# Kernel optimization log

Hardware: AMD Instinct MI355X
Metric: run time of the kernel (lower is better)

## Reference

```python
import jax, jax.numpy as jnp
import numpy as np

N, E, H, NH = 10000, 160000, 128, 8
HD = H // NH
LDIM = 8  # (lmax+1)**2 - 1 with lmax=2
CUTOFF = 5.0


def setup_inputs() -> dict:
    key = jax.random.key(0)
    ks = jax.random.split(key, 20)
    w = lambda k, shape: jax.random.normal(k, shape, jnp.float32) * 0.05
    return dict(
        node_feats=jax.random.normal(ks[0], (N, H), jnp.float32),
        edge_feats=jax.random.normal(ks[1], (E, H), jnp.float32),
        vector_feats=jax.random.normal(ks[2], (N, LDIM, H), jnp.float32),
        distances=jax.random.uniform(ks[3], (E,), jnp.float32) * CUTOFF,
        d_ij=jax.random.normal(ks[4], (E, LDIM), jnp.float32),
        senders=jax.random.randint(ks[5], (E,), 0, N),
        receivers=jax.random.randint(ks[6], (E,), 0, N),
        ln_scale=jnp.ones((H,), jnp.float32),
        ln_bias=jnp.zeros((H,), jnp.float32),
        vln_w=jnp.ones((H,), jnp.float32),
        W_vec=w(ks[7], (H, 3 * H)),
        Wq=w(ks[8], (H, H)), bq=jnp.zeros((H,), jnp.float32),
        Wk=w(ks[9], (H, H)), bk=jnp.zeros((H,), jnp.float32),
        Wv=w(ks[10], (H, H)), bv=jnp.zeros((H,), jnp.float32),
        Wdk=w(ks[11], (H, H)), bdk=jnp.zeros((H,), jnp.float32),
        Wdv=w(ks[12], (H, H)), bdv=jnp.zeros((H,), jnp.float32),
        Ws=w(ks[13], (H, 2 * H)), bs=jnp.zeros((2 * H,), jnp.float32),
        Wo=w(ks[14], (H, 3 * H)), bo=jnp.zeros((3 * H,), jnp.float32),
        Wf=w(ks[15], (H, H)), bf=jnp.zeros((H,), jnp.float32),
        Wsrc=w(ks[16], (H, H)),
        Wtrg=w(ks[17], (H, H)),
    )


def _reject(vec, d):
    # vector rejection of vec [E, L, H] against direction d [E, L]
    proj = (vec * d[:, :, None]).sum(axis=1, keepdims=True)
    return vec - proj * d[:, :, None]


def _forward(node_feats, edge_feats, vector_feats, distances, d_ij, senders, receivers,
             ln_scale, ln_bias, vln_w, W_vec, Wq, bq, Wk, bk, Wv, bv, Wdk, bdk, Wdv, bdv,
             Ws, bs, Wo, bo, Wf, bf, Wsrc, Wtrg):
    silu = jax.nn.silu
    n = node_feats.shape[0]
    # LayerNorm (eps=1e-5) on node feats
    mu = node_feats.mean(-1, keepdims=True)
    xc = node_feats - mu
    var = (xc * xc).mean(-1, keepdims=True)
    x = xc * jax.lax.rsqrt(var + 1e-5) * ln_scale + ln_bias
    # VecLayerNorm with norm_type='none' -> identity norm + learned per-channel scale
    vec = vector_feats * vln_w
    q = (x @ Wq + bq).reshape(-1, NH, HD)
    k = (x @ Wk + bk).reshape(-1, NH, HD)
    v = (x @ Wv + bv).reshape(-1, NH, HD)
    dk = silu(edge_feats @ Wdk + bdk).reshape(-1, NH, HD)
    dv = silu(edge_feats @ Wdv + bdv).reshape(-1, NH, HD)
    vec1, vec2, vec3 = jnp.split(vec @ W_vec, [H, 2 * H], axis=-1)
    vec_dot = (vec1 * vec2).sum(axis=1)  # [N, H]
    # per-edge gathers
    q_i = q[receivers]
    k_j = k[senders]
    v_j = v[senders]
    vec_j = vec[senders]  # [E, LDIM, H]
    # attention-style message with cosine cutoff
    cut = 0.5 * (jnp.cos(distances * (jnp.pi / CUTOFF)) + 1.0) * (distances < CUTOFF)
    attn = silu((q_i * k_j * dk).sum(-1)) * cut[:, None]  # [E, NH]
    vj = ((v_j * dv) * attn[:, :, None]).reshape(-1, H)   # [E, H]
    s1, s2 = jnp.split(silu(vj @ Ws + bs), [H], axis=1)
    vec_msg = vec_j * s1[:, None, :] + s2[:, None, :] * d_ij[:, :, None]
    # scatter reduce to nodes
    node_agg = jax.ops.segment_sum(vj, receivers, num_segments=n)
    vec_agg = jax.ops.segment_sum(vec_msg, receivers, num_segments=n)
    o1, o2, o3 = jnp.split(node_agg @ Wo + bo, [H, 2 * H], axis=1)
    dx = vec_dot * o2 + o3
    dvec = vec3 * o1[:, None, :] + vec_agg
    # edge update (last_layer=False)
    w1 = _reject(vec[receivers] @ Wtrg, d_ij)
    w2 = _reject(vec_j @ Wsrc, -d_ij)
    w_dot = (w1 * w2).sum(axis=1)  # [E, H]
    df_ij = silu(edge_feats @ Wf + bf) * w_dot
    return dx, df_ij, dvec


def reference(node_feats, edge_feats, vector_feats, distances, d_ij, senders, receivers,
              ln_scale, ln_bias, vln_w, W_vec, Wq, bq, Wk, bk, Wv, bv, Wdk, bdk, Wdv, bdv,
              Ws, bs, Wo, bo, Wf, bf, Wsrc, Wtrg):
    return _forward(node_feats, edge_feats, vector_feats, distances, d_ij, senders, receivers,
                    ln_scale, ln_bias, vln_w, W_vec, Wq, bq, Wk, bk, Wv, bv, Wdk, bdk, Wdv, bdv,
                    Ws, bs, Wo, bo, Wf, bf, Wsrc, Wtrg)
```

## Files before the change

### kernel.cpp

```cpp
#include <hip/hip_runtime.h>
#include <math.h>

#define NN 10000
#define NE 160000
#define H  128
#define LD 8

typedef unsigned short ushort_t;
typedef short bf16x8 __attribute__((ext_vector_type(8)));
typedef float f32x4 __attribute__((ext_vector_type(4)));

__device__ __forceinline__ float silu_f(float x){ return x / (1.0f + expf(-x)); }
__device__ __forceinline__ float4 f4z(){ return make_float4(0.f,0.f,0.f,0.f); }

__device__ __forceinline__ void fma4(float4& acc, float s, const float4 w){
    acc.x = fmaf(s, w.x, acc.x);
    acc.y = fmaf(s, w.y, acc.y);
    acc.z = fmaf(s, w.z, acc.z);
    acc.w = fmaf(s, w.w, acc.w);
}

__device__ __forceinline__ float4 silu4(float4 a, float4 b){
    return make_float4(silu_f(a.x+b.x), silu_f(a.y+b.y), silu_f(a.z+b.z), silu_f(a.w+b.w));
}

__device__ __forceinline__ ushort_t f2bf(float f){
    union { float f; unsigned int u; } x; x.f = f;
    unsigned int r = x.u + 0x7FFFu + ((x.u >> 16) & 1u);
    return (ushort_t)(r >> 16);
}
__device__ __forceinline__ unsigned int pack2bf(float a, float b){
    return (unsigned int)f2bf(a) | ((unsigned int)f2bf(b) << 16);
}
__device__ __forceinline__ float bf2f_hi(unsigned int u){
    union { unsigned int u; float f; } x; x.u = u & 0xffff0000u; return x.f;
}
__device__ __forceinline__ float bf2f_lo(unsigned int u){
    union { unsigned int u; float f; } x; x.u = u << 16; return x.f;
}

__global__ void k_prepw(const float* __restrict__ Wdk, const float* __restrict__ Wdv,
                        const float* __restrict__ Ws,
                        ushort_t* __restrict__ wdkT, ushort_t* __restrict__ wdvT,
                        ushort_t* __restrict__ wsT){
    int i = blockIdx.x * 256 + threadIdx.x;
    if (i < 128*128){
        int n = i >> 7, kk = i & 127;
        wdkT[n*128 + kk] = f2bf(Wdk[kk*128 + n]);
        wdvT[n*128 + kk] = f2bf(Wdv[kk*128 + n]);
    }
    if (i < 256*128){
        int n = i >> 7, kk = i & 127;
        wsT[n*128 + kk] = f2bf(Ws[kk*256 + n]);
    }
}

__global__ void k_ef2bf(const float* __restrict__ ef, ushort_t* __restrict__ ef_bf){
    size_t i = (size_t)blockIdx.x * 256 + threadIdx.x;
    const float4* s = (const float4*)ef;
    float4 a = s[2*i], b = s[2*i+1];
    uint4 u;
    u.x = pack2bf(a.x, a.y); u.y = pack2bf(a.z, a.w);
    u.z = pack2bf(b.x, b.y); u.w = pack2bf(b.z, b.w);
    ((uint4*)ef_bf)[i] = u;
}

__global__ void k_hist(const int* __restrict__ rcv, int* __restrict__ cnt){
    int e = blockIdx.x * 256 + threadIdx.x;
    if (e < NE) atomicAdd(&cnt[rcv[e]], 1);
}

__global__ __launch_bounds__(256) void k_scan(const int* __restrict__ cnt, int* __restrict__ offs){
    __shared__ int part[256];
    const int t = threadIdx.x;
    const int CH = 40;
    int loc[CH];
    int base = t * CH;
    int lsum = 0;
    if (base < NN){
        #pragma unroll
        for (int i = 0; i < CH; i++){ loc[i] = cnt[base + i]; lsum += loc[i]; }
    }
    part[t] = lsum;
    __syncthreads();
    for (int off = 1; off < 256; off <<= 1){
        int v = (t >= off) ? part[t - off] : 0;
        __syncthreads();
        part[t] += v;
        __syncthreads();
    }
    int ex = part[t] - lsum;
    if (base < NN){
        int run = ex;
        #pragma unroll
        for (int i = 0; i < CH; i++){ offs[base + i] = run; run += loc[i]; }
    }
    if (t == 255) offs[NN] = part[255];
}

__global__ void k_scatter(const int* __restrict__ rcv, const int* __restrict__ offs,
                          int* __restrict__ cnt2, int* __restrict__ eidx){
    int e = blockIdx.x * 256 + threadIdx.x;
    if (e < NE){
        int r = rcv[e];
        int p = atomicAdd(&cnt2[r], 1);
        eidx[offs[r] + p] = e;
    }
}

__global__ __launch_bounds__(128) void node_pre(
    const float* __restrict__ nf, const float* __restrict__ vf,
    const float* __restrict__ ln_s, const float* __restrict__ ln_b,
    const float* __restrict__ vlnw, const float* __restrict__ W_vec,
    const float* __restrict__ Wq, const float* __restrict__ bq,
    const float* __restrict__ Wk, const float* __restrict__ bk,
    const float* __restrict__ Wv, const float* __restrict__ bv,
    const float* __restrict__ Wtrg, const float* __restrict__ Wsrc,
    float* __restrict__ q, float* __restrict__ k, float* __restrict__ v,
    ushort_t* __restrict__ vec_bf, float* __restrict__ vdot, float* __restrict__ vec3,
    ushort_t* __restrict__ Vt, ushort_t* __restrict__ Vs)
{
    const int n = blockIdx.x;
    const int h = threadIdx.x;
    __shared__ float x_s[H];
    __shared__ float vec_s[LD][H];
    __shared__ float red[4];

    float xv = nf[(size_t)n*H + h];
    float s1 = xv, s2 = xv*xv;
    #pragma unroll
    for (int o = 32; o >= 1; o >>= 1){
        s1 += __shfl_xor(s1, o, 64);
        s2 += __shfl_xor(s2, o, 64);
    }
    const int wid = h >> 6;
    if ((h & 63) == 0){ red[wid] = s1; red[2+wid] = s2; }
    __syncthreads();
    float mean = (red[0] + red[1]) * (1.0f/H);
    float var  = (red[2] + red[3]) * (1.0f/H) - mean*mean;
    float x = (xv - mean) * rsqrtf(var + 1e-5f) * ln_s[h] + ln_b[h];
    x_s[h] = x;
    float w = vlnw[h];
    #pragma unroll
    for (int l = 0; l < LD; l++){
        size_t i = ((size_t)n*LD + l)*H + h;
        float t = vf[i] * w;
        vec_s[l][h] = t;
        vec_bf[i] = f2bf(t);
    }
    __syncthreads();

    float aq = bq[h], ak = bk[h], av = bv[h];
    float a1[LD], a2[LD], a3[LD], at[LD], as_[LD];
    #pragma unroll
    for (int l = 0; l < LD; l++){ a1[l]=0.f; a2[l]=0.f; a3[l]=0.f; at[l]=0.f; as_[l]=0.f; }

    for (int kk = 0; kk < H; kk++){
        float xk = x_s[kk];
        aq = fmaf(xk, Wq[kk*H + h], aq);
        ak = fmaf(xk, Wk[kk*H + h], ak);
        av = fmaf(xk, Wv[kk*H + h], av);
        float w1 = W_vec[kk*(3*H) + h];
        float w2 = W_vec[kk*(3*H) + H + h];
        float w3 = W_vec[kk*(3*H) + 2*H + h];
        float wt = Wtrg[kk*H + h];
        float ws = Wsrc[kk*H + h];
        #pragma unroll
        for (int l = 0; l < LD; l++){
            float vk = vec_s[l][kk];
            a1[l] = fmaf(vk, w1, a1[l]);
            a2[l] = fmaf(vk, w2, a2[l]);
            a3[l] = fmaf(vk, w3, a3[l]);
            at[l] = fmaf(vk, wt, at[l]);
            as_[l]= fmaf(vk, ws, as_[l]);
        }
    }
    q[(size_t)n*H + h] = aq;
    k[(size_t)n*H + h] = ak;
    v[(size_t)n*H + h] = av;
    float vd = 0.f;
    #pragma unroll
    for (int l = 0; l < LD; l++) vd = fmaf(a1[l], a2[l], vd);
    vdot[(size_t)n*H + h] = vd;
    #pragma unroll
    for (int l = 0; l < LD; l++){
        size_t i = ((size_t)n*LD + l)*H + h;
        vec3[i] = a3[l];
        Vt[i]   = f2bf(at[l]);
        Vs[i]   = f2bf(as_[l]);
    }
}

__global__ __launch_bounds__(256) void edge_attn(
    const ushort_t* __restrict__ ef_bf,
    const ushort_t* __restrict__ wdkT, const float* __restrict__ bdk,
    const ushort_t* __restrict__ wdvT, const float* __restrict__ bdv,
    const int* __restrict__ snd, const int* __restrict__ rcv,
    const float* __restrict__ dist,
    const float* __restrict__ q, const float* __restrict__ k, const float* __restrict__ v,
    ushort_t* __restrict__ vj)
{
    __shared__ ushort_t dk_s[64][136];
    __shared__ ushort_t dv_s[64][136];

    const int tid  = threadIdx.x;
    const int lane = tid & 63;
    const int m0   = (tid >> 6) * 16;
    const size_t e0 = (size_t)blockIdx.x * 64;

    const int mrow = lane & 15;
    const int kblk = lane >> 4;

    f32x4 accK[8], accV[8];
    #pragma unroll
    for (int nt = 0; nt < 8; nt++){ accK[nt] = (f32x4)(0.f); accV[nt] = (f32x4)(0.f); }

    const ushort_t* Arow = ef_bf + (e0 + m0 + mrow)*H + kblk*8;
    const ushort_t* wkb  = wdkT + (size_t)mrow*H + kblk*8;
    const ushort_t* wvb  = wdvT + (size_t)mrow*H + kblk*8;

    #pragma unroll
    for (int ks = 0; ks < 4; ks++){
        bf16x8 a = *(const bf16x8*)(Arow + ks*32);
        #pragma unroll
        for (int nt = 0; nt < 8; nt++){
            bf16x8 bk8 = *(const bf16x8*)(wkb + (size_t)nt*16*H + ks*32);
            accK[nt] = __builtin_amdgcn_mfma_f32_16x16x32_bf16(a, bk8, accK[nt], 0, 0, 0);
            bf16x8 bv8 = *(const bf16x8*)(wvb + (size_t)nt*16*H + ks*32);
            accV[nt] = __builtin_amdgcn_mfma_f32_16x16x32_bf16(a, bv8, accV[nt], 0, 0, 0);
        }
    }

    const int lrow = m0 + 4*kblk;
    #pragma unroll
    for (int nt = 0; nt < 8; nt++){
        int coln = nt*16 + mrow;
        float bkn = bdk[coln], bvn = bdv[coln];
        #pragma unroll
        for (int r = 0; r < 4; r++){
            dk_s[lrow + r][coln] = f2bf(silu_f(accK[nt][r] + bkn));
            dv_s[lrow + r][coln] = f2bf(silu_f(accV[nt][r] + bvn));
        }
    }
    __syncthreads();

    const int r  = tid >> 2, cq = tid & 3;
    const size_t e = e0 + r;
    const int s  = snd[e], rr = rcv[e];
    const float d = dist[e];
    const float cut = (d < 5.0f) ? 0.5f*(cosf(d*0.6283185307179586f) + 1.0f) : 0.0f;
    const float* qrow = q + (size_t)rr*H + cq*32;
    const float* krow = k + (size_t)s*H + cq*32;
    const float* vrow = v + (size_t)s*H + cq*32;
    ushort_t* vjrow = vj + e*H + cq*32;

    #pragma unroll
    for (int hh = 0; hh < 2; hh++){
        const int c0 = hh*16;
        float p = 0.f;
        #pragma unroll
        for (int j = 0; j < 4; j++){
            float4 q4 = *(const float4*)(qrow + c0 + 4*j);
            float4 k4 = *(const float4*)(krow + c0 + 4*j);
            uint2 du = *(const uint2*)&dk_s[r][cq*32 + c0 + 4*j];
            p += q4.x*k4.x*bf2f_lo(du.x) + q4.y*k4.y*bf2f_hi(du.x)
               + q4.z*k4.z*bf2f_lo(du.y) + q4.w*k4.w*bf2f_hi(du.y);
        }
        float attn = silu_f(p) * cut;
        #pragma unroll
        for (int j = 0; j < 4; j++){
            float4 v4 = *(const float4*)(vrow + c0 + 4*j);
            uint2 du = *(const uint2*)&dv_s[r][cq*32 + c0 + 4*j];
            uint2 u;
            u.x = pack2bf(v4.x*bf2f_lo(du.x)*attn, v4.y*bf2f_hi(du.x)*attn);
            u.y = pack2bf(v4.z*bf2f_lo(du.y)*attn, v4.w*bf2f_hi(du.y)*attn);
            *(uint2*)(vjrow + c0 + 4*j) = u;
        }
    }
}

__global__ __launch_bounds__(256) void edge_s(
    const ushort_t* __restrict__ vj, const ushort_t* __restrict__ wsT,
    const float* __restrict__ bs, ushort_t* __restrict__ s12)
{
    __shared__ ushort_t s_s[64][264];

    const int tid  = threadIdx.x;
    const int lane = tid & 63;
    const int m0   = (tid >> 6) * 16;
    const size_t e0 = (size_t)blockIdx.x * 64;

    const int mrow = lane & 15;
    const int kblk = lane >> 4;

    f32x4 acc[16];
    #pragma unroll
    for (int nt = 0; nt < 16; nt++) acc[nt] = (f32x4)(0.f);

    const ushort_t* Arow = vj + (e0 + m0 + mrow)*H + kblk*8;
    const ushort_t* wb   = wsT + (size_t)mrow*H + kblk*8;

    #pragma unroll
    for (int ks = 0; ks < 4; ks++){
        bf16x8 a = *(const bf16x8*)(Arow + ks*32);
        #pragma unroll
        for (int nt = 0; nt < 16; nt++){
            bf16x8 b8 = *(const bf16x8*)(wb + (size_t)nt*16*H + ks*32);
            acc[nt] = __builtin_amdgcn_mfma_f32_16x16x32_bf16(a, b8, acc[nt], 0, 0, 0);
        }
    }

    const int lrow = m0 + 4*kblk;
    #pragma unroll
    for (int nt = 0; nt < 16; nt++){
        int coln = nt*16 + mrow;
        float bb = bs[coln];
        #pragma unroll
        for (int r = 0; r < 4; r++)
            s_s[lrow + r][coln] = f2bf(silu_f(acc[nt][r] + bb));
    }
    __syncthreads();

    const int r = tid >> 2, cq = tid & 3;
    const uint4* srcp = (const uint4*)&s_s[r][cq*64];
    uint4* dstp = (uint4*)&s12[(e0 + r)*256 + cq*64];
    #pragma unroll
    for (int j = 0; j < 8; j++) dstp[j] = srcp[j];
}

__global__ __launch_bounds__(256) void edge_df(
    const float* __restrict__ ef, const float* __restrict__ Wf, const float* __restrict__ bf_,
    const int* __restrict__ eidx,
    const int* __restrict__ snd, const int* __restrict__ rcv,
    const float* __restrict__ dij,
    const ushort_t* __restrict__ Vt, const ushort_t* __restrict__ Vs,
    float* __restrict__ df)
{
    __shared__ float wf_s[H][64];
    __shared__ float e_s[16][H];
    __shared__ int   eidx_s[16];
    __shared__ int   snd_s[16];
    __shared__ int   rcv_s[16];
    __shared__ float dij_s[16][LD];

    const int tid = threadIdx.x;
    const int by = blockIdx.y;
    const int p0 = blockIdx.x * 16;

    if (tid < 16) eidx_s[tid] = eidx[p0 + tid];
    __syncthreads();

    for (int i = tid; i < H*16; i += 256){
        int row = i >> 4, c4 = i & 15;
        *(float4*)&wf_s[row][c4*4] = *(const float4*)&Wf[row*H + by*64 + c4*4];
    }
    for (int i = tid; i < 16*32; i += 256){
        int row = i >> 5, c4 = i & 31;
        *(float4*)&e_s[row][c4*4] = *(const float4*)&ef[(size_t)eidx_s[row]*H + c4*4];
    }
    if (tid < 16){ snd_s[tid] = snd[eidx_s[tid]]; rcv_s[tid] = rcv[eidx_s[tid]]; }
    if (tid < 16*LD){
        int row = tid >> 3, l = tid & 7;
        dij_s[row][l] = dij[(size_t)eidx_s[row]*LD + l];
    }
    __syncthreads();

    const int g = tid & 15, r0 = tid >> 4;
    float4 af = f4z();
    for (int kk = 0; kk < H; kk++){
        float4 w4 = *(float4*)&wf_s[kk][g*4];
        fma4(af, e_s[r0][kk], w4);
    }
    float4 bf4 = *(const float4*)&bf_[by*64 + g*4];
    float4 f4 = silu4(af, bf4);

    const int e = eidx_s[r0];
    const int s = snd_s[r0], rr = rcv_s[r0];
    const ushort_t* Ar = Vt + ((size_t)rr*LD)*H + by*64 + g*4;
    const ushort_t* Br = Vs + ((size_t)s*LD)*H + by*64 + g*4;

    float4 AB = f4z(), aa = f4z(), bb = f4z();
    float dd = 0.f;
    #pragma unroll
    for (int l = 0; l < LD; l++){
        float dl = dij_s[r0][l];
        dd = fmaf(dl, dl, dd);
        uint2 ua = *(const uint2*)&Ar[(size_t)l*H];
        uint2 ub = *(const uint2*)&Br[(size_t)l*H];
        float Ax = bf2f_lo(ua.x), Ay = bf2f_hi(ua.x), Az = bf2f_lo(ua.y), Aw = bf2f_hi(ua.y);
        float Bx = bf2f_lo(ub.x), By = bf2f_hi(ub.x), Bz = bf2f_lo(ub.y), Bw = bf2f_hi(ub.y);
        AB.x = fmaf(Ax, Bx, AB.x); AB.y = fmaf(Ay, By, AB.y);
        AB.z = fmaf(Az, Bz, AB.z); AB.w = fmaf(Aw, Bw, AB.w);
        aa.x = fmaf(Ax, dl, aa.x); aa.y = fmaf(Ay, dl, aa.y);
        aa.z = fmaf(Az, dl, aa.z); aa.w = fmaf(Aw, dl, aa.w);
        bb.x = fmaf(Bx, dl, bb.x); bb.y = fmaf(By, dl, bb.y);
        bb.z = fmaf(Bz, dl, bb.z); bb.w = fmaf(Bw, dl, bb.w);
    }
    float c = 2.0f - dd;
    float4 o = make_float4(f4.x*(AB.x - aa.x*bb.x*c),
                           f4.y*(AB.y - aa.y*bb.y*c),
                           f4.z*(AB.z - aa.z*bb.z*c),
                           f4.w*(AB.w - aa.w*bb.w*c));
    *(float4*)&df[(size_t)e*H + by*64 + g*4] = o;
}

__global__ __launch_bounds__(128) void node_gather(
    const int* __restrict__ offs, const int* __restrict__ eidx, const int* __restrict__ snd,
    const ushort_t* __restrict__ vj, const ushort_t* __restrict__ s12,
    const float* __restrict__ dij, const ushort_t* __restrict__ vec,
    const float* __restrict__ Wo, const float* __restrict__ bo,
    const float* __restrict__ vdot, const float* __restrict__ vec3,
    float* __restrict__ dx, float* __restrict__ dvec)
{
    const int n = blockIdx.x, h = threadIdx.x;
    const int beg = offs[n], end = offs[n+1];
    float na = 0.f;
    float av[LD];
    #pragma unroll
    for (int l = 0; l < LD; l++) av[l] = 0.f;

    for (int i = beg; i < end; i++){
        int e = eidx[i];
        int s = snd[e];
        float vjv = bf2f_lo((unsigned int)vj[(size_t)e*H + h]);
        float s1 = bf2f_lo((unsigned int)s12[(size_t)e*256 + h]);
        float s2 = bf2f_lo((unsigned int)s12[(size_t)e*256 + 128 + h]);
        na += vjv;
        float4 d0 = *(const float4*)&dij[(size_t)e*LD];
        float4 d1 = *(const float4*)&dij[(size_t)e*LD + 4];
        const ushort_t* vr = &vec[(size_t)s*LD*H + h];
        av[0] = fmaf(bf2f_lo((unsigned int)vr[0*H]), s1, fmaf(d0.x, s2, av[0]));
        av[1] = fmaf(bf2f_lo((unsigned int)vr[1*H]), s1, fmaf(d0.y, s2, av[1]));
        av[2] = fmaf(bf2f_lo((unsigned int)vr[2*H]), s1, fmaf(d0.z, s2, av[2]));
        av[3] = fmaf(bf2f_lo((unsigned int)vr[3*H]), s1, fmaf(d0.w, s2, av[3]));
        av[4] = fmaf(bf2f_lo((unsigned int)vr[4*H]), s1, fmaf(d1.x, s2, av[4]));
        av[5] = fmaf(bf2f_lo((unsigned int)vr[5*H]), s1, fmaf(d1.y, s2, av[5]));
        av[6] = fmaf(bf2f_lo((unsigned int)vr[6*H]), s1, fmaf(d1.z, s2, av[6]));
        av[7] = fmaf(bf2f_lo((unsigned int)vr[7*H]), s1, fmaf(d1.w, s2, av[7]));
    }

    __shared__ float na_s[H];
    na_s[h] = na;
    __syncthreads();
    float o1 = bo[h], o2 = bo[H + h], o3 = bo[2*H + h];
    for (int kk = 0; kk < H; kk++){
        float a = na_s[kk];
        o1 = fmaf(a, Wo[kk*(3*H) + h], o1);
        o2 = fmaf(a, Wo[kk*(3*H) + H + h], o2);
        o3 = fmaf(a, Wo[kk*(3*H) + 2*H + h], o3);
    }
    dx[(size_t)n*H + h] = fmaf(vdot[(size_t)n*H + h], o2, o3);
    #pragma unroll
    for (int l = 0; l < LD; l++){
        size_t i2 = ((size_t)n*LD + l)*H + h;
        dvec[i2] = fmaf(vec3[i2], o1, av[l]);
    }
}

extern "C" void kernel_launch(void* const* d_in, const int* in_sizes, int n_in,
                              void* d_out, int out_size, void* d_ws, size_t ws_size,
                              hipStream_t stream) {
    const float* nf    = (const float*)d_in[0];
    const float* ef    = (const float*)d_in[1];
    const float* vf    = (const float*)d_in[2];
    const float* dist  = (const float*)d_in[3];
    const float* dij   = (const float*)d_in[4];
    const int*   snd   = (const int*)d_in[5];
    const int*   rcv   = (const int*)d_in[6];
    const float* ln_s  = (const float*)d_in[7];
    const float* ln_b  = (const float*)d_in[8];
    const float* vlnw  = (const float*)d_in[9];
    const float* W_vec = (const float*)d_in[10];
    const float* Wq    = (const float*)d_in[11];
    const float* bq    = (const float*)d_in[12];
    const float* Wk    = (const float*)d_in[13];
    const float* bk    = (const float*)d_in[14];
    const float* Wv    = (const float*)d_in[15];
    const float* bv    = (const float*)d_in[16];
    const float* Wdk   = (const float*)d_in[17];
    const float* bdk   = (const float*)d_in[18];
    const float* Wdv   = (const float*)d_in[19];
    const float* bdv   = (const float*)d_in[20];
    const float* Ws    = (const float*)d_in[21];
    const float* bs    = (const float*)d_in[22];
    const float* Wo    = (const float*)d_in[23];
    const float* bo    = (const float*)d_in[24];
    const float* Wf    = (const float*)d_in[25];
    const float* bf_   = (const float*)d_in[26];
    const float* Wsrc  = (const float*)d_in[27];
    const float* Wtrg  = (const float*)d_in[28];

    float* out  = (float*)d_out;
    float* dx   = out;
    float* df   = out + (size_t)NN*H;
    float* dvec = df + (size_t)NE*H;

    float* w = (float*)d_ws;
    size_t off = 0;
    float* q    = w + off; off += (size_t)NN*H;
    float* k    = w + off; off += (size_t)NN*H;
    float* v    = w + off; off += (size_t)NN*H;
    float* vdot = w + off; off += (size_t)NN*H;
    float* vec3 = w + off; off += (size_t)NN*LD*H;
    ushort_t* vec_bf = (ushort_t*)(w + off); off += (size_t)NN*LD*H/2;
    ushort_t* Vt     = (ushort_t*)(w + off); off += (size_t)NN*LD*H/2;
    ushort_t* Vs     = (ushort_t*)(w + off); off += (size_t)NN*LD*H/2;
    ushort_t* vj     = (ushort_t*)(w + off); off += (size_t)NE*H/2;
    ushort_t* s12    = (ushort_t*)(w + off); off += (size_t)NE*256/2;
    ushort_t* ef_bf  = s12;
    ushort_t* wdkT = (ushort_t*)(w + off); off += 128*128/2;
    ushort_t* wdvT = (ushort_t*)(w + off); off += 128*128/2;
    ushort_t* wsT  = (ushort_t*)(w + off); off += 256*128/2;
    int* cnt  = (int*)(w + off); off += NN;
    int* cnt2 = (int*)(w + off); off += NN;
    int* offs = (int*)(w + off); off += NN + 1;
    int* eidx = (int*)(w + off); off += NE;

    hipMemsetAsync(cnt,  0, NN*sizeof(int), stream);
    hipMemsetAsync(cnt2, 0, NN*sizeof(int), stream);

    k_prepw<<<128, 256, 0, stream>>>(Wdk, Wdv, Ws, wdkT, wdvT, wsT);
    k_ef2bf<<<NE*H/8/256, 256, 0, stream>>>(ef, ef_bf);

    k_hist<<<(NE+255)/256, 256, 0, stream>>>(rcv, cnt);
    k_scan<<<1, 256, 0, stream>>>(cnt, offs);
    k_scatter<<<(NE+255)/256, 256, 0, stream>>>(rcv, offs, cnt2, eidx);

    node_pre<<<NN, 128, 0, stream>>>(nf, vf, ln_s, ln_b, vlnw, W_vec,
                                     Wq, bq, Wk, bk, Wv, bv, Wtrg, Wsrc,
                                     q, k, v, vec_bf, vdot, vec3, Vt, Vs);

    edge_attn<<<NE/64, 256, 0, stream>>>(ef_bf, wdkT, bdk, wdvT, bdv, snd, rcv, dist,
                                         q, k, v, vj);

    edge_df<<<dim3(NE/16, 2), 256, 0, stream>>>(ef, Wf, bf_, eidx, snd, rcv, dij, Vt, Vs, df);

    edge_s<<<NE/64, 256, 0, stream>>>(vj, wsT, bs, s12);

    node_gather<<<NN, 128, 0, stream>>>(offs, eidx, snd, vj, s12, dij, vec_bf,
                                        Wo, bo, vdot, vec3, dx, dvec);
}
```

Baseline: 910.7 us.

## Split node_pre into LayerNorm plus bf16 MFMA GEMMs for QKV and vector projections

Replaces the per-node scalar FP32 projection kernel with a LayerNorm/scaling kernel that emits bf16, followed by two MFMA GEMM kernels: one for Q/K/V and one for the concatenated W_vec/Wtrg/Wsrc projections, with weights pre-transposed to bf16. The vdot reduction is computed from MFMA accumulators via a lane shuffle, and vec3 is stored as bf16 through a shared-memory staging tile. This removes the heavy scalar FMA loop that re-read weights from global memory for every node. In exchange it lowers Q/K/V and vec3 precision to bf16 and adds extra kernel launches.

```diff
diff --git a/kernel.cpp b/kernel.cpp
--- a/kernel.cpp
+++ b/kernel.cpp
@@ -39,19 +39,38 @@
     union { unsigned int u; float f; } x; x.u = u << 16; return x.f;
 }
 
-__global__ void k_prepw(const float* __restrict__ Wdk, const float* __restrict__ Wdv,
+__global__ void k_prepw(const float* __restrict__ Wq, const float* __restrict__ Wk,
+                        const float* __restrict__ Wv, const float* __restrict__ W_vec,
+                        const float* __restrict__ Wtrg, const float* __restrict__ Wsrc,
+                        const float* __restrict__ Wdk, const float* __restrict__ Wdv,
                         const float* __restrict__ Ws,
+                        ushort_t* __restrict__ wqkvT, ushort_t* __restrict__ wvecT,
                         ushort_t* __restrict__ wdkT, ushort_t* __restrict__ wdvT,
                         ushort_t* __restrict__ wsT){
     int i = blockIdx.x * 256 + threadIdx.x;
-    if (i < 128*128){
-        int n = i >> 7, kk = i & 127;
-        wdkT[n*128 + kk] = f2bf(Wdk[kk*128 + n]);
-        wdvT[n*128 + kk] = f2bf(Wdv[kk*128 + n]);
-    }
-    if (i < 256*128){
-        int n = i >> 7, kk = i & 127;
-        wsT[n*128 + kk] = f2bf(Ws[kk*256 + n]);
+    int n = i >> 7, kk = i & 127;
+    if (n < 384){
+        float v;
+        if (n < 128)      v = Wq[kk*128 + n];
+        else if (n < 256) v = Wk[kk*128 + (n-128)];
+        else              v = Wv[kk*128 + (n-256)];
+        wqkvT[n*128 + kk] = f2bf(v);
+    } else if (n < 1024){
+        int m = n - 384;
+        float v;
+        if (m < 384)      v = W_vec[kk*384 + m];
+        else if (m < 512) v = Wtrg[kk*128 + (m-384)];
+        else              v = Wsrc[kk*128 + (m-512)];
+        wvecT[m*128 + kk] = f2bf(v);
+    } else if (n < 1152){
+        int m = n - 1024;
+        wdkT[m*128 + kk] = f2bf(Wdk[kk*128 + m]);
+    } else if (n < 1280){
+        int m = n - 1152;
+        wdvT[m*128 + kk] = f2bf(Wdv[kk*128 + m]);
+    } else if (n < 1536){
+        int m = n - 1280;
+        wsT[m*128 + kk] = f2bf(Ws[kk*256 + m]);
     }
 }
 
@@ -108,24 +127,14 @@
     }
 }
 
-__global__ __launch_bounds__(128) void node_pre(
+__global__ __launch_bounds__(128) void node_ln(
     const float* __restrict__ nf, const float* __restrict__ vf,
     const float* __restrict__ ln_s, const float* __restrict__ ln_b,
-    const float* __restrict__ vlnw, const float* __restrict__ W_vec,
-    const float* __restrict__ Wq, const float* __restrict__ bq,
-    const float* __restrict__ Wk, const float* __restrict__ bk,
-    const float* __restrict__ Wv, const float* __restrict__ bv,
-    const float* __restrict__ Wtrg, const float* __restrict__ Wsrc,
-    float* __restrict__ q, float* __restrict__ k, float* __restrict__ v,
-    ushort_t* __restrict__ vec_bf, float* __restrict__ vdot, float* __restrict__ vec3,
-    ushort_t* __restrict__ Vt, ushort_t* __restrict__ Vs)
+    const float* __restrict__ vlnw,
+    ushort_t* __restrict__ x_bf, ushort_t* __restrict__ vec_bf)
 {
-    const int n = blockIdx.x;
-    const int h = threadIdx.x;
-    __shared__ float x_s[H];
-    __shared__ float vec_s[LD][H];
+    const int n = blockIdx.x, h = threadIdx.x;
     __shared__ float red[4];
-
     float xv = nf[(size_t)n*H + h];
     float s1 = xv, s2 = xv*xv;
     #pragma unroll
@@ -139,55 +148,124 @@
     float mean = (red[0] + red[1]) * (1.0f/H);
     float var  = (red[2] + red[3]) * (1.0f/H) - mean*mean;
     float x = (xv - mean) * rsqrtf(var + 1e-5f) * ln_s[h] + ln_b[h];
-    x_s[h] = x;
+    x_bf[(size_t)n*H + h] = f2bf(x);
     float w = vlnw[h];
     #pragma unroll
     for (int l = 0; l < LD; l++){
         size_t i = ((size_t)n*LD + l)*H + h;
-        float t = vf[i] * w;
-        vec_s[l][h] = t;
-        vec_bf[i] = f2bf(t);
-    }
-    __syncthreads();
-
-    float aq = bq[h], ak = bk[h], av = bv[h];
-    float a1[LD], a2[LD], a3[LD], at[LD], as_[LD];
-    #pragma unroll
-    for (int l = 0; l < LD; l++){ a1[l]=0.f; a2[l]=0.f; a3[l]=0.f; at[l]=0.f; as_[l]=0.f; }
-
-    for (int kk = 0; kk < H; kk++){
-        float xk = x_s[kk];
-        aq = fmaf(xk, Wq[kk*H + h], aq);
-        ak = fmaf(xk, Wk[kk*H + h], ak);
-        av = fmaf(xk, Wv[kk*H + h], av);
-        float w1 = W_vec[kk*(3*H) + h];
-        float w2 = W_vec[kk*(3*H) + H + h];
-        float w3 = W_vec[kk*(3*H) + 2*H + h];
-        float wt = Wtrg[kk*H + h];
-        float ws = Wsrc[kk*H + h];
-        #pragma unroll
-        for (int l = 0; l < LD; l++){
-            float vk = vec_s[l][kk];
-            a1[l] = fmaf(vk, w1, a1[l]);
-            a2[l] = fmaf(vk, w2, a2[l]);
-            a3[l] = fmaf(vk, w3, a3[l]);
-            at[l] = fmaf(vk, wt, at[l]);
-            as_[l]= fmaf(vk, ws, as_[l]);
-        }
-    }
-    q[(size_t)n*H + h] = aq;
-    k[(size_t)n*H + h] = ak;
-    v[(size_t)n*H + h] = av;
-    float vd = 0.f;
-    #pragma unroll
-    for (int l = 0; l < LD; l++) vd = fmaf(a1[l], a2[l], vd);
-    vdot[(size_t)n*H + h] = vd;
-    #pragma unroll
-    for (int l = 0; l < LD; l++){
-        size_t i = ((size_t)n*LD + l)*H + h;
-        vec3[i] = a3[l];
-        Vt[i]   = f2bf(at[l]);
-        Vs[i]   = f2bf(as_[l]);
+        vec_bf[i] = f2bf(vf[i] * w);
+    }
+}
+
+__global__ __launch_bounds__(256) void node_qkv(
+    const ushort_t* __restrict__ x_bf, const ushort_t* __restrict__ wqkvT,
+    const float* __restrict__ bq, const float* __restrict__ bk, const float* __restrict__ bv,
+    float* __restrict__ q, float* __restrict__ k, float* __restrict__ v)
+{
+    const int tid  = threadIdx.x;
+    const int lane = tid & 63;
+    const int m0   = (tid >> 6) * 16;
+    const int e0   = blockIdx.x * 64;
+
+    const int mrow = lane & 15;
+    const int kblk = lane >> 4;
+
+    f32x4 acc[24];
+    #pragma unroll
+    for (int nt = 0; nt < 24; nt++) acc[nt] = (f32x4)(0.f);
+
+    int arow = e0 + m0 + mrow; if (arow >= NN) arow = NN-1;
+    const ushort_t* Arow = x_bf + (size_t)arow*H + kblk*8;
+    const ushort_t* wb   = wqkvT + (size_t)mrow*H + kblk*8;
+
+    #pragma unroll
+    for (int ks = 0; ks < 4; ks++){
+        bf16x8 a = *(const bf16x8*)(Arow + ks*32);
+        #pragma unroll
+        for (int nt = 0; nt < 24; nt++){
+            bf16x8 b8 = *(const bf16x8*)(wb + (size_t)nt*16*H + ks*32);
+            acc[nt] = __builtin_amdgcn_mfma_f32_16x16x32_bf16(a, b8, acc[nt], 0, 0, 0);
+        }
+    }
+    float* outs[3] = {q, k, v};
+    const float* bias[3] = {bq, bk, bv};
+    #pragma unroll
+    for (int g = 0; g < 3; g++){
+        #pragma unroll
+        for (int t = 0; t < 8; t++){
+            int col = t*16 + mrow;
+            float bb = bias[g][col];
+            #pragma unroll
+            for (int r = 0; r < 4; r++){
+                int row = e0 + m0 + kblk*4 + r;
+                if (row < NN) outs[g][(size_t)row*H + col] = acc[g*8+t][r] + bb;
+            }
+        }
+    }
+}
+
+__global__ __launch_bounds__(256) void node_vec(
+    const ushort_t* __restrict__ vec_bf, const ushort_t* __restrict__ wvecT,
+    float* __restrict__ vdot, ushort_t* __restrict__ vec3,
+    ushort_t* __restrict__ Vt, ushort_t* __restrict__ Vs)
+{
+    __shared__ ushort_t st_s[64][136];
+
+    const int tid  = threadIdx.x;
+    const int lane = tid & 63;
+    const int wv   = tid >> 6;
+    const int m0   = wv * 16;
+    const size_t r0 = (size_t)blockIdx.x * 64;
+
+    const int mrow = lane & 15;
+    const int kblk = lane >> 4;
+
+    f32x4 acc[40];
+    #pragma unroll
+    for (int nt = 0; nt < 40; nt++) acc[nt] = (f32x4)(0.f);
+
+    const ushort_t* Arow = vec_bf + (r0 + m0 + mrow)*H + kblk*8;
+    const ushort_t* wb   = wvecT + (size_t)mrow*H + kblk*8;
+
+    #pragma unroll
+    for (int ks = 0; ks < 4; ks++){
+        bf16x8 a = *(const bf16x8*)(Arow + ks*32);
+        #pragma unroll
+        for (int nt = 0; nt < 40; nt++){
+            bf16x8 b8 = *(const bf16x8*)(wb + (size_t)nt*16*H + ks*32);
+            acc[nt] = __builtin_amdgcn_mfma_f32_16x16x32_bf16(a, b8, acc[nt], 0, 0, 0);
+        }
+    }
+
+    #pragma unroll
+    for (int t = 0; t < 8; t++){
+        float p = acc[t][0]*acc[t+8][0] + acc[t][1]*acc[t+8][1]
+                + acc[t][2]*acc[t+8][2] + acc[t][3]*acc[t+8][3];
+        p += __shfl_xor(p, 16, 64);
+        if ((kblk & 1) == 0){
+            int node = (int)(r0 >> 3) + wv*2 + (kblk >> 1);
+            vdot[(size_t)node*H + t*16 + mrow] = p;
+        }
+    }
+
+    ushort_t* outs[3] = {vec3, Vt, Vs};
+    #pragma unroll
+    for (int g = 0; g < 3; g++){
+        __syncthreads();
+        #pragma unroll
+        for (int t = 0; t < 8; t++){
+            int coln = t*16 + mrow;
+            int lr = m0 + kblk*4;
+            st_s[lr+0][coln] = f2bf(acc[16+g*8+t][0]);
+            st_s[lr+1][coln] = f2bf(acc[16+g*8+t][1]);
+            st_s[lr+2][coln] = f2bf(acc[16+g*8+t][2]);
+            st_s[lr+3][coln] = f2bf(acc[16+g*8+t][3]);
+        }
+        __syncthreads();
+        const int rr = tid >> 2, qq = tid & 3;
+        uint4* dst = (uint4*)&outs[g][(r0 + rr)*H + qq*32];
+        const uint4* src = (const uint4*)&st_s[rr][qq*32];
+        dst[0] = src[0]; dst[1] = src[1]; dst[2] = src[2]; dst[3] = src[3];
     }
 }
 
@@ -409,7 +487,7 @@
     const ushort_t* __restrict__ vj, const ushort_t* __restrict__ s12,
     const float* __restrict__ dij, const ushort_t* __restrict__ vec,
     const float* __restrict__ Wo, const float* __restrict__ bo,
-    const float* __restrict__ vdot, const float* __restrict__ vec3,
+    const float* __restrict__ vdot, const ushort_t* __restrict__ vec3,
     float* __restrict__ dx, float* __restrict__ dvec)
 {
     const int n = blockIdx.x, h = threadIdx.x;
@@ -453,7 +531,7 @@
     #pragma unroll
     for (int l = 0; l < LD; l++){
         size_t i2 = ((size_t)n*LD + l)*H + h;
-        dvec[i2] = fmaf(vec3[i2], o1, av[l]);
+        dvec[i2] = fmaf(bf2f_lo((unsigned int)vec3[i2]), o1, av[l]);
     }
 }
 
@@ -501,16 +579,19 @@
     float* k    = w + off; off += (size_t)NN*H;
     float* v    = w + off; off += (size_t)NN*H;
     float* vdot = w + off; off += (size_t)NN*H;
-    float* vec3 = w + off; off += (size_t)NN*LD*H;
+    ushort_t* x_bf   = (ushort_t*)(w + off); off += (size_t)NN*H/2;
     ushort_t* vec_bf = (ushort_t*)(w + off); off += (size_t)NN*LD*H/2;
+    ushort_t* vec3   = (ushort_t*)(w + off); off += (size_t)NN*LD*H/2;
     ushort_t* Vt     = (ushort_t*)(w + off); off += (size_t)NN*LD*H/2;
     ushort_t* Vs     = (ushort_t*)(w + off); off += (size_t)NN*LD*H/2;
     ushort_t* vj     = (ushort_t*)(w + off); off += (size_t)NE*H/2;
     ushort_t* s12    = (ushort_t*)(w + off); off += (size_t)NE*256/2;
     ushort_t* ef_bf  = s12;
-    ushort_t* wdkT = (ushort_t*)(w + off); off += 128*128/2;
-    ushort_t* wdvT = (ushort_t*)(w + off); off += 128*128/2;
-    ushort_t* wsT  = (ushort_t*)(w + off); off += 256*128/2;
+    ushort_t* wqkvT = (ushort_t*)(w + off); off += 384*128/2;
+    ushort_t* wvecT = (ushort_t*)(w + off); off += 640*128/2;
+    ushort_t* wdkT  = (ushort_t*)(w + off); off += 128*128/2;
+    ushort_t* wdvT  = (ushort_t*)(w + off); off += 128*128/2;
+    ushort_t* wsT   = (ushort_t*)(w + off); off += 256*128/2;
     int* cnt  = (int*)(w + off); off += NN;
     int* cnt2 = (int*)(w + off); off += NN;
     int* offs = (int*)(w + off); off += NN + 1;
@@ -519,16 +600,19 @@
     hipMemsetAsync(cnt,  0, NN*sizeof(int), stream);
     hipMemsetAsync(cnt2, 0, NN*sizeof(int), stream);
 
-    k_prepw<<<128, 256, 0, stream>>>(Wdk, Wdv, Ws, wdkT, wdvT, wsT);
+    k_prepw<<<768, 256, 0, stream>>>(Wq, Wk, Wv, W_vec, Wtrg, Wsrc, Wdk, Wdv, Ws,
+                                     wqkvT, wvecT, wdkT, wdvT, wsT);
     k_ef2bf<<<NE*H/8/256, 256, 0, stream>>>(ef, ef_bf);
 
     k_hist<<<(NE+255)/256, 256, 0, stream>>>(rcv, cnt);
     k_scan<<<1, 256, 0, stream>>>(cnt, offs);
     k_scatter<<<(NE+255)/256, 256, 0, stream>>>(rcv, offs, cnt2, eidx);
 
-    node_pre<<<NN, 128, 0, stream>>>(nf, vf, ln_s, ln_b, vlnw, W_vec,
-                                     Wq, bq, Wk, bk, Wv, bv, Wtrg, Wsrc,
-                                     q, k, v, vec_bf, vdot, vec3, Vt, Vs);
+    node_ln<<<NN, 128, 0, stream>>>(nf, vf, ln_s, ln_b, vlnw, x_bf, vec_bf);
+
+    node_qkv<<<(NN+63)/64, 256, 0, stream>>>(x_bf, wqkvT, bq, bk, bv, q, k, v);
+
+    node_vec<<<NN*LD/64, 256, 0, stream>>>(vec_bf, wvecT, vdot, vec3, Vt, Vs);
 
     edge_attn<<<NE/64, 256, 0, stream>>>(ef_bf, wdkT, bdk, wdvT, bdv, snd, rcv, dist,
                                          q, k, v, vj);
```

Measured after the change: 838.3 us. -8.0%, faster.
